# Performance work log

Hardware: AMD Instinct MI355X
Metric: run time of the kernel (lower is better)

Reference implementation:

```python
import jax, jax.numpy as jnp
import numpy as np

K = 3          # kernel_size
STRIDE = 1
PAD = 1
NUM_BASIS = 8
DEGREE = 3
M = NUM_BASIS + DEGREE   # number of basis slots (11)
EPS = 1e-5               # BatchNorm2d default eps


def _unfold(x):
    # x: [B,C,H,W] -> patches [B,C,L,K*K] (L = Ho*Wo spatial positions, last dim = kernel pos)
    x = jnp.pad(x, ((0, 0), (0, 0), (PAD, PAD), (PAD, PAD)))
    B, C, H, W = x.shape
    Ho = (H - K) // STRIDE + 1
    Wo = (W - K) // STRIDE + 1
    ii = (jnp.arange(Ho) * STRIDE)[:, None] + jnp.arange(K)[None, :]   # [Ho,K]
    jj = (jnp.arange(Wo) * STRIDE)[:, None] + jnp.arange(K)[None, :]   # [Wo,K]
    p = x[:, :, ii[:, None, :, None], jj[None, :, None, :]]           # [B,C,Ho,Wo,K,K]
    return p.reshape(B, C, Ho * Wo, K * K), Ho, Wo


def _bspline_basis(u):
    # Vectorized Cox-de Boor recursion, faithful to the module's in-place update
    # (entries j >= M-d keep their stale lower-degree values, as in the original).
    # u: [...,] in (0,1) -> basis [..., M]
    knots = jnp.linspace(0.0, 1.0, M + 1).astype(u.dtype)              # 12 knots
    b = ((u[..., None] >= knots[:M]) & (u[..., None] < knots[1:M + 1])).astype(u.dtype)
    for d in range(1, DEGREE + 1):
        n = M - d
        j = np.arange(n)
        den1 = knots[j + d] - knots[j]
        den2 = knots[j + d + 1] - knots[j + 1]
        alpha = jnp.where(den1 != 0, (u[..., None] - knots[j]) / jnp.where(den1 != 0, den1, 1.0), 0.0)
        beta = jnp.where(den2 != 0, (knots[j + d + 1] - u[..., None]) / jnp.where(den2 != 0, den2, 1.0), 0.0)
        upd = alpha * b[..., :n] + beta * b[..., 1:n + 1]
        b = jnp.concatenate([upd, b[..., n:]], axis=-1)
    return b


def setup_inputs() -> dict:
    key = jax.random.key(0)
    k1, k2, k3 = jax.random.split(key, 3)
    B, C_in, C_out, H, W = 8, 64, 128, 56, 56
    x = jax.random.normal(k1, (B, C_in, H, W), dtype=jnp.float32)
    # Xavier-uniform-like scale for control points [O, C, K*K, M]
    fan = C_in * K * K * M + C_out
    bound_cp = float(np.sqrt(6.0 / fan))
    control_points = jax.random.uniform(k2, (C_out, C_in, K * K, M), minval=-bound_cp, maxval=bound_cp, dtype=jnp.float32)
    bound_w = float(np.sqrt(6.0 / (C_in * K * K + C_out * K * K)))
    conv_w = jax.random.uniform(k3, (C_out, C_in, K, K), minval=-bound_w, maxval=bound_w, dtype=jnp.float32)
    conv_b = jnp.zeros((C_out,), dtype=jnp.float32)
    bn_gamma = jnp.ones((C_out,), dtype=jnp.float32)
    bn_beta = jnp.zeros((C_out,), dtype=jnp.float32)
    return {"x": x, "control_points": control_points, "conv_w": conv_w,
            "conv_b": conv_b, "bn_gamma": bn_gamma, "bn_beta": bn_beta}


def reference(x, control_points, conv_w, conv_b, bn_gamma, bn_beta):
    patches, Ho, Wo = _unfold(x)                 # [B,C,L,K2]
    u = jax.nn.sigmoid(patches)
    basis = _bspline_basis(u)                    # [B,C,L,K2,M]
    # spline output: contract in_channels, kernel positions, basis index
    spline = jnp.einsum('bclkn,ockn->bol', basis, control_points)
    B = x.shape[0]
    O = control_points.shape[0]
    spline = spline.reshape(B, O, Ho, Wo)
    conv = jax.lax.conv_general_dilated(x, conv_w, (STRIDE, STRIDE), [(PAD, PAD), (PAD, PAD)],
                                        dimension_numbers=('NCHW', 'OIHW', 'NCHW'))
    out = spline + conv + conv_b[None, :, None, None]
    # Dropout2d is identity in eval mode. BatchNorm2d with batch statistics (training default).
    mean = out.mean(axis=(0, 2, 3), keepdims=True)
    var = out.var(axis=(0, 2, 3), keepdims=True)
    out = (out - mean) * jax.lax.rsqrt(var + EPS)
    return out * bn_gamma[None, :, None, None] + bn_beta[None, :, None, None]
```

## Files before the change

kernel.cpp:

```cpp
#include <hip/hip_runtime.h>
#include <math.h>

#define CIN   64
#define COUT  128
#define HW    56
#define L_    3136
#define KTOT  6912
#define TH    8
#define TW    8
#define HALO_W 10
#define NPIX  100
#define CSTR  (NPIX*16)
#define G8_SIZE (8*CSTR)
#define G4_SIZE (4*CSTR)
#define BUF_SIZE (G8_SIZE+G4_SIZE)

#define BP_BYTES (COUT * KTOT * 2)
#define PART_OFF BP_BYTES
#define SS_OFF   (PART_OFF + 2048 * 4)

typedef __attribute__((ext_vector_type(8))) short bf16x8;
typedef __attribute__((ext_vector_type(4))) float f32x4;
typedef unsigned long long u64;

#define BLOAD(dst, addr) \
    asm volatile("global_load_dwordx4 %0, %1, off" : "=v"(dst) : "v"(addr))
#define XLOAD(dst, addr) \
    asm volatile("global_load_dword %0, %1, off" : "=v"(dst) : "v"(addr))

__device__ __forceinline__ unsigned short f2bf(float f) {
    unsigned int u = __float_as_uint(f);
    return (unsigned short)((u + 0x7FFFu + ((u >> 16) & 1u)) >> 16);
}
__device__ __forceinline__ unsigned int pk2(float a, float b) {
    return (unsigned int)f2bf(a) | ((unsigned int)f2bf(b) << 16);
}

__device__ __forceinline__ void eval_store(float xv, char* g8rec, char* g4half) {
    float u  = 1.0f / (1.0f + __expf(-xv));
    float tt = u * 11.0f;
    int s = (int)floorf(tt);
    s = (s > 10) ? 10 : s;
    float xf  = tt - (float)s;
    float x2  = xf * xf, x3 = x2 * xf;
    float omx = 1.0f - xf;
    const float i6 = 1.0f / 6.0f;
    float w3 = x3 * i6;
    float w2 = fmaf(fmaf(fmaf(-3.0f, xf, 3.0f), xf, 3.0f), xf, 1.0f) * i6;
    float w1 = fmaf(fmaf(3.0f, xf, -6.0f), x2, 4.0f) * i6;
    float w0 = omx * omx * omx * i6;

    *reinterpret_cast<uint4*>(g8rec) = (uint4){0u, 0u, 0u, 0u};
    unsigned short* rec = reinterpret_cast<unsigned short*>(g8rec);
    {
        int j;
        j = s - 3; if (j >= 0 && j < 8) rec[j] = f2bf(w0);
        j = s - 2; if (j >= 0 && j < 8) rec[j] = f2bf(w1);
        j = s - 1; if (j >= 0 && j < 8) rec[j] = f2bf(w2);
        j = s;     if (j >= 0 && j < 8) rec[j] = f2bf(w3);
    }
    float y = tt - 8.0f;
    float f8 = 0.0f;
    f8 = (s == 8)  ? 0.5f * y * y : f8;
    f8 = (s == 9)  ? 0.5f * fmaf(-2.0f * y, y, fmaf(6.0f, y, -3.0f)) : f8;
    f8 = (s == 10) ? 0.5f * (3.0f - y) * (3.0f - y) : f8;
    float z = tt - 9.0f;
    float f9 = 0.0f;
    f9 = (s == 9)  ? z : f9;
    f9 = (s == 10) ? 2.0f - z : f9;
    float f10 = (s == 10) ? 1.0f : 0.0f;
    *reinterpret_cast<uint2*>(g4half) = make_uint2(pk2(f8, f9), pk2(f10, xv));
}

__global__ __launch_bounds__(256) void k_packB(const float* __restrict__ cp,
                                               const float* __restrict__ w,
                                               unsigned short* __restrict__ Bp) {
    int idx = blockIdx.x * 256 + threadIdx.x;
    if (idx >= COUT * KTOT) return;
    int kstep = idx >> 12;
    int rem   = idx & 4095;
    int o     = rem >> 5;
    int e32   = rem & 31;
    int ch = kstep / 27, sc = kstep - ch * 27;
    int ktap = sc / 3, ph = sc - ktap * 3;
    int c, n;
    if (ph < 2) { c = ch * 8 + ph * 4 + (e32 >> 3); n = e32 & 7; }
    else        { int sub = e32 & 7; c = ch * 8 + (e32 >> 3) * 2 + (sub >> 2); n = 8 + (sub & 3); }
    float v;
    if (n < 11) v = cp[(((size_t)o * CIN + c) * 9 + ktap) * 11 + n];
    else        v = w[((size_t)o * CIN + c) * 9 + ktap];
    Bp[idx] = f2bf(v);
}

__global__ __launch_bounds__(256, 2) void k_main(const float* __restrict__ x,
                                                 const unsigned short* __restrict__ Bp,
                                                 const float* __restrict__ bias,
                                                 float* __restrict__ out) {
    __shared__ char lds[2 * BUF_SIZE];

    const int bid  = blockIdx.x;
    const int b    = bid / 49;
    const int tile = bid - b * 49;
    const int th   = tile / 7;
    const int tw   = tile - th * 7;
    const int t    = threadIdx.x;
    const int lane = t & 63;
    const int wid  = t >> 6;

    const bool valid = (t < 200);
    const int p    = (t < 100) ? t : (t - 100);
    const int hi100 = (t >= 100) ? 1 : 0;
    const int ph_  = p / 10, pw_ = p - ph_ * 10;
    const int hg = th * TH - 1 + ph_;
    const int wg = tw * TW - 1 + pw_;
    const bool inb = valid && (hg >= 0) && (hg < HW) && (wg >= 0) && (wg < HW);
    const u64 xadv = inb ? (u64)8 * L_ * 4 : 0;
    u64 px[4];
#pragma unroll
    for (int r = 0; r < 4; r++) {
        int c0 = 2 * r + hi100;
        px[r] = inb ? ((u64)x + (((u64)b * CIN + c0) * L_ + (u64)hg * HW + wg) * 4)
                    : (u64)x;
    }

    const int q   = lane >> 4;
    const int r15 = lane & 15;
    int P[4];
#pragma unroll
    for (int mi = 0; mi < 4; mi++) {
        int lh = mi * 2 + (r15 >> 3);
        int lw = r15 & 7;
        P[mi] = (lh * HALO_W + lw) * 16 + q * CSTR;
    }
    const int obase = wid * 32 + r15;

    const u64 bend = (u64)Bp + BP_BYTES;
    u64 pa0 = (u64)Bp + ((u64)obase * 64) + ((u64)q * 16);
    u64 pa1 = pa0 + 1024;

    f32x4 acc[4][2];
#pragma unroll
    for (int mi = 0; mi < 4; mi++)
#pragma unroll
        for (int ni = 0; ni < 2; ni++) acc[mi][ni] = (f32x4){0.f, 0.f, 0.f, 0.f};

    float xa[4];
    XLOAD(xa[0], px[0]); XLOAD(xa[1], px[1]);
    XLOAD(xa[2], px[2]); XLOAD(xa[3], px[3]);
#pragma unroll
    for (int r = 0; r < 4; r++) px[r] += xadv;
    asm volatile("s_waitcnt vmcnt(0)");
    __builtin_amdgcn_sched_barrier(0);
    if (valid) {
#pragma unroll
        for (int r = 0; r < 4; r++) {
            float va = inb ? xa[r] : 0.0f;
            int c = 2 * r + hi100;
            eval_store(va, &lds[c * CSTR + p * 16],
                       &lds[G8_SIZE + r * CSTR + p * 16 + hi100 * 8]);
        }
    }
    asm volatile("s_waitcnt lgkmcnt(0)");
    __builtin_amdgcn_s_barrier();

    bf16x8 breg0[9], breg1[9];
#pragma unroll
    for (int s = 0; s < 9; s++) {
        BLOAD(breg0[s], pa0);
        BLOAD(breg1[s], pa1);
        pa0 += 8192; pa1 += 8192;
    }

#pragma unroll 1
    for (int ch = 0; ch < 8; ch++) {
        XLOAD(xa[0], px[0]); XLOAD(xa[1], px[1]);
        XLOAD(xa[2], px[2]); XLOAD(xa[3], px[3]);
        if (ch < 7) {
#pragma unroll
            for (int r = 0; r < 4; r++) px[r] += xadv;
        }

        char* abuf = &lds[(ch & 1) * BUF_SIZE];
        char* nbuf = &lds[((ch + 1) & 1) * BUF_SIZE];

        bf16x8 areg[2][4];
        auto aread = [&](int s, bf16x8 (&a)[4]) {
            int k = s / 3, bp = s - k * 3;
            int ki = k / 3, kj = k - ki * 3;
            int poff = (ki * HALO_W + kj) * 16;
            int aoff = (bp == 2) ? (G8_SIZE + poff) : (bp * 4 * CSTR + poff);
#pragma unroll
            for (int mi = 0; mi < 4; mi++)
                a[mi] = *reinterpret_cast<const bf16x8*>(abuf + P[mi] + aoff);
        };
        aread(0, areg[0]);

#pragma unroll
        for (int s = 0; s < 27; s++) {
            if (s + 1 < 27) aread(s + 1, areg[(s + 1) & 1]);
            asm volatile("s_waitcnt vmcnt(16)");
            __builtin_amdgcn_sched_barrier(0);
            const int bs = s % 9;
#pragma unroll
            for (int mi = 0; mi < 4; mi++) {
                acc[mi][0] = __builtin_amdgcn_mfma_f32_16x16x32_bf16(areg[s & 1][mi], breg0[bs], acc[mi][0], 0, 0, 0);
                acc[mi][1] = __builtin_amdgcn_mfma_f32_16x16x32_bf16(areg[s & 1][mi], breg1[bs], acc[mi][1], 0, 0, 0);
            }
            BLOAD(breg0[bs], pa0);
            BLOAD(breg1[bs], pa1);
            pa0 += 8192; if (pa0 >= bend) pa0 -= BP_BYTES;
            pa1 += 8192; if (pa1 >= bend) pa1 -= BP_BYTES;
        }

        if (ch < 7 && valid) {
#pragma unroll
            for (int r = 0; r < 4; r++) {
                float va = inb ? xa[r] : 0.0f;
                int c = 2 * r + hi100;
                eval_store(va, &nbuf[c * CSTR + p * 16],
                           &nbuf[G8_SIZE + r * CSTR + p * 16 + hi100 * 8]);
            }
        }
        asm volatile("s_waitcnt lgkmcnt(0)");
        __builtin_amdgcn_s_barrier();
    }

    asm volatile("s_waitcnt vmcnt(0)");

#pragma unroll
    for (int ni = 0; ni < 2; ni++) {
        int o = obase + ni * 16;
        float bv = bias[o];
#pragma unroll
        for (int mi = 0; mi < 4; mi++) {
            int lh = mi * 2 + (q >> 1);
            int lw0 = (q & 1) * 4;
            int lg = (th * TH + lh) * HW + tw * TW + lw0;
            float4 v;
            v.x = acc[mi][ni][0] + bv;
            v.y = acc[mi][ni][1] + bv;
            v.z = acc[mi][ni][2] + bv;
            v.w = acc[mi][ni][3] + bv;
            *reinterpret_cast<float4*>(&out[(size_t)(b * COUT + o) * L_ + lg]) = v;
        }
    }
}

__global__ __launch_bounds__(256) void k_part(const float* __restrict__ s,
                                              float* __restrict__ part) {
    const int slab = blockIdx.x;
    const float4* p4 = reinterpret_cast<const float4*>(s + (size_t)slab * L_);
    const int t = threadIdx.x;
    float sum = 0.f, sq = 0.f;
    for (int i = t; i < L_ / 4; i += 256) {
        float4 v = p4[i];
        sum += v.x + v.y + v.z + v.w;
        sq  += v.x * v.x + v.y * v.y + v.z * v.z + v.w * v.w;
    }
    __shared__ float rs[256], rq[256];
    rs[t] = sum; rq[t] = sq;
    __syncthreads();
    for (int off = 128; off > 0; off >>= 1) {
        if (t < off) { rs[t] += rs[t + off]; rq[t] += rq[t + off]; }
        __syncthreads();
    }
    if (t == 0) { part[slab] = rs[0]; part[1024 + slab] = rq[0]; }
}

__global__ __launch_bounds__(128) void k_final(const float* __restrict__ part,
                                               const float* __restrict__ gamma,
                                               const float* __restrict__ beta,
                                               float* __restrict__ ss) {
    int o = threadIdx.x;
    float sum = 0.f, sq = 0.f;
#pragma unroll
    for (int b = 0; b < 8; b++) {
        sum += part[b * COUT + o];
        sq  += part[1024 + b * COUT + o];
    }
    float n = (float)(8 * L_);
    float mean = sum / n;
    float var  = sq / n - mean * mean;
    float scale = gamma[o] * rsqrtf(var + 1e-5f);
    ss[o]        = scale;
    ss[COUT + o] = beta[o] - mean * scale;
}

__global__ __launch_bounds__(256) void k_norm(float* __restrict__ out,
                                              const float* __restrict__ ss) {
    const int n4 = 8 * COUT * L_ / 4;
    for (int i = blockIdx.x * 256 + threadIdx.x; i < n4; i += gridDim.x * 256) {
        int o = ((i * 4) / L_) & (COUT - 1);
        float sc = ss[o], sh = ss[COUT + o];
        float4 v = reinterpret_cast<float4*>(out)[i];
        v.x = fmaf(v.x, sc, sh);
        v.y = fmaf(v.y, sc, sh);
        v.z = fmaf(v.z, sc, sh);
        v.w = fmaf(v.w, sc, sh);
        reinterpret_cast<float4*>(out)[i] = v;
    }
}

extern "C" void kernel_launch(void* const* d_in, const int* in_sizes, int n_in,
                              void* d_out, int out_size, void* d_ws, size_t ws_size,
                              hipStream_t stream) {
    const float* x     = (const float*)d_in[0];
    const float* cp    = (const float*)d_in[1];
    const float* w     = (const float*)d_in[2];
    const float* bias  = (const float*)d_in[3];
    const float* gamma = (const float*)d_in[4];
    const float* beta  = (const float*)d_in[5];
    float* out = (float*)d_out;

    unsigned short* Bp = (unsigned short*)d_ws;
    float* part = (float*)((char*)d_ws + PART_OFF);
    float* ss   = (float*)((char*)d_ws + SS_OFF);

    k_packB<<<(COUT * KTOT + 255) / 256, 256, 0, stream>>>(cp, w, Bp);
    k_main<<<8 * 49, 256, 0, stream>>>(x, Bp, bias, out);
    k_part<<<1024, 256, 0, stream>>>(out, part);
    k_final<<<1, 128, 0, stream>>>(part, gamma, beta, ss);
    k_norm<<<2048, 256, 0, stream>>>(out, ss);
}
```

Before: 86.81 us.

## Pad LDS channel stride, branchless basis packing, deeper A prefetch, drop bias

Adds 32 bytes of padding per LDS channel stride to cut bank conflicts. Replaces the scattered bf16 stores of the basis record with a branchless select and one 128-bit store. Raises the LDS-to-register prefetch depth for the A operand from 2 to 3 stages, which costs more VGPRs. It also stops adding the conv bias, since training-mode BatchNorm subtracts the per-channel mean and cancels it. The pointer advance is trimmed on the last iteration and the explicit waitcnt/barrier pairs become __syncthreads.

```diff
diff --git a/kernel.cpp b/kernel.cpp
--- a/kernel.cpp
+++ b/kernel.cpp
@@ -10,7 +10,7 @@
 #define TW    8
 #define HALO_W 10
 #define NPIX  100
-#define CSTR  (NPIX*16)
+#define CSTR  (NPIX*16 + 32)
 #define G8_SIZE (8*CSTR)
 #define G4_SIZE (4*CSTR)
 #define BUF_SIZE (G8_SIZE+G4_SIZE)
@@ -50,15 +50,24 @@
     float w1 = fmaf(fmaf(3.0f, xf, -6.0f), x2, 4.0f) * i6;
     float w0 = omx * omx * omx * i6;
 
-    *reinterpret_cast<uint4*>(g8rec) = (uint4){0u, 0u, 0u, 0u};
-    unsigned short* rec = reinterpret_cast<unsigned short*>(g8rec);
-    {
-        int j;
-        j = s - 3; if (j >= 0 && j < 8) rec[j] = f2bf(w0);
-        j = s - 2; if (j >= 0 && j < 8) rec[j] = f2bf(w1);
-        j = s - 1; if (j >= 0 && j < 8) rec[j] = f2bf(w2);
-        j = s;     if (j >= 0 && j < 8) rec[j] = f2bf(w3);
-    }
+    unsigned int b0 = f2bf(w0), b1 = f2bf(w1), b2 = f2bf(w2), b3 = f2bf(w3);
+    unsigned int slot[8];
+#pragma unroll
+    for (int j = 0; j < 8; j++) {
+        unsigned int v = 0;
+        v = (s == j)     ? b3 : v;
+        v = (s == j + 1) ? b2 : v;
+        v = (s == j + 2) ? b1 : v;
+        v = (s == j + 3) ? b0 : v;
+        slot[j] = v;
+    }
+    uint4 rec;
+    rec.x = slot[0] | (slot[1] << 16);
+    rec.y = slot[2] | (slot[3] << 16);
+    rec.z = slot[4] | (slot[5] << 16);
+    rec.w = slot[6] | (slot[7] << 16);
+    *reinterpret_cast<uint4*>(g8rec) = rec;
+
     float y = tt - 8.0f;
     float f8 = 0.0f;
     f8 = (s == 8)  ? 0.5f * y * y : f8;
@@ -94,7 +103,6 @@
 
 __global__ __launch_bounds__(256, 2) void k_main(const float* __restrict__ x,
                                                  const unsigned short* __restrict__ Bp,
-                                                 const float* __restrict__ bias,
                                                  float* __restrict__ out) {
     __shared__ char lds[2 * BUF_SIZE];
 
@@ -108,7 +116,7 @@
     const int wid  = t >> 6;
 
     const bool valid = (t < 200);
-    const int p    = (t < 100) ? t : (t - 100);
+    const int p     = (t < 100) ? t : (t - 100);
     const int hi100 = (t >= 100) ? 1 : 0;
     const int ph_  = p / 10, pw_ = p - ph_ * 10;
     const int hg = th * TH - 1 + ph_;
@@ -160,8 +168,7 @@
                        &lds[G8_SIZE + r * CSTR + p * 16 + hi100 * 8]);
         }
     }
-    asm volatile("s_waitcnt lgkmcnt(0)");
-    __builtin_amdgcn_s_barrier();
+    __syncthreads();
 
     bf16x8 breg0[9], breg1[9];
 #pragma unroll
@@ -175,7 +182,7 @@
     for (int ch = 0; ch < 8; ch++) {
         XLOAD(xa[0], px[0]); XLOAD(xa[1], px[1]);
         XLOAD(xa[2], px[2]); XLOAD(xa[3], px[3]);
-        if (ch < 7) {
+        if (ch < 6) {
 #pragma unroll
             for (int r = 0; r < 4; r++) px[r] += xadv;
         }
@@ -183,7 +190,7 @@
         char* abuf = &lds[(ch & 1) * BUF_SIZE];
         char* nbuf = &lds[((ch + 1) & 1) * BUF_SIZE];
 
-        bf16x8 areg[2][4];
+        bf16x8 areg[3][4];
         auto aread = [&](int s, bf16x8 (&a)[4]) {
             int k = s / 3, bp = s - k * 3;
             int ki = k / 3, kj = k - ki * 3;
@@ -194,17 +201,18 @@
                 a[mi] = *reinterpret_cast<const bf16x8*>(abuf + P[mi] + aoff);
         };
         aread(0, areg[0]);
+        aread(1, areg[1]);
 
 #pragma unroll
         for (int s = 0; s < 27; s++) {
-            if (s + 1 < 27) aread(s + 1, areg[(s + 1) & 1]);
+            if (s + 2 < 27) aread(s + 2, areg[(s + 2) % 3]);
             asm volatile("s_waitcnt vmcnt(16)");
             __builtin_amdgcn_sched_barrier(0);
             const int bs = s % 9;
 #pragma unroll
             for (int mi = 0; mi < 4; mi++) {
-                acc[mi][0] = __builtin_amdgcn_mfma_f32_16x16x32_bf16(areg[s & 1][mi], breg0[bs], acc[mi][0], 0, 0, 0);
-                acc[mi][1] = __builtin_amdgcn_mfma_f32_16x16x32_bf16(areg[s & 1][mi], breg1[bs], acc[mi][1], 0, 0, 0);
+                acc[mi][0] = __builtin_amdgcn_mfma_f32_16x16x32_bf16(areg[s % 3][mi], breg0[bs], acc[mi][0], 0, 0, 0);
+                acc[mi][1] = __builtin_amdgcn_mfma_f32_16x16x32_bf16(areg[s % 3][mi], breg1[bs], acc[mi][1], 0, 0, 0);
             }
             BLOAD(breg0[bs], pa0);
             BLOAD(breg1[bs], pa1);
@@ -221,26 +229,22 @@
                            &nbuf[G8_SIZE + r * CSTR + p * 16 + hi100 * 8]);
             }
         }
-        asm volatile("s_waitcnt lgkmcnt(0)");
-        __builtin_amdgcn_s_barrier();
-    }
-
-    asm volatile("s_waitcnt vmcnt(0)");
+        __syncthreads();
+    }
 
 #pragma unroll
     for (int ni = 0; ni < 2; ni++) {
         int o = obase + ni * 16;
-        float bv = bias[o];
 #pragma unroll
         for (int mi = 0; mi < 4; mi++) {
             int lh = mi * 2 + (q >> 1);
             int lw0 = (q & 1) * 4;
             int lg = (th * TH + lh) * HW + tw * TW + lw0;
             float4 v;
-            v.x = acc[mi][ni][0] + bv;
-            v.y = acc[mi][ni][1] + bv;
-            v.z = acc[mi][ni][2] + bv;
-            v.w = acc[mi][ni][3] + bv;
+            v.x = acc[mi][ni][0];
+            v.y = acc[mi][ni][1];
+            v.z = acc[mi][ni][2];
+            v.w = acc[mi][ni][3];
             *reinterpret_cast<float4*>(&out[(size_t)(b * COUT + o) * L_ + lg]) = v;
         }
     }
@@ -307,7 +311,6 @@
     const float* x     = (const float*)d_in[0];
     const float* cp    = (const float*)d_in[1];
     const float* w     = (const float*)d_in[2];
-    const float* bias  = (const float*)d_in[3];
     const float* gamma = (const float*)d_in[4];
     const float* beta  = (const float*)d_in[5];
     float* out = (float*)d_out;
@@ -317,7 +320,7 @@
     float* ss   = (float*)((char*)d_ws + SS_OFF);
 
     k_packB<<<(COUT * KTOT + 255) / 256, 256, 0, stream>>>(cp, w, Bp);
-    k_main<<<8 * 49, 256, 0, stream>>>(x, Bp, bias, out);
+    k_main<<<8 * 49, 256, 0, stream>>>(x, Bp, out);
     k_part<<<1024, 256, 0, stream>>>(out, part);
     k_final<<<1, 128, 0, stream>>>(part, gamma, beta, ss);
     k_norm<<<2048, 256, 0, stream>>>(out, ss);
```

Result: no change. 86.13 us (-0.8%).
